# Kernel tuning notes

Measured on AMD Instinct MI355X. Metric: run time of the kernel, lower is better.

The kernel has to match this reference:

```python
import jax, jax.numpy as jnp
import numpy as np

N = 100000   # nodes
E = 1600000  # edges
IN = 32      # in_channels
H = 64       # hidden_channels
L = 16       # latent_dim
G = 64       # graphs in batch


def setup_inputs() -> dict:
    key = jax.random.key(0)
    ks = jax.random.split(key, 20)
    def w(k, shape, fan):
        return jax.random.normal(k, shape, jnp.float32) * (1.0 / np.sqrt(fan))
    inp = {}
    inp["x"] = jax.random.normal(ks[0], (N, IN), jnp.float32)
    inp["edge_index"] = jax.random.randint(ks[1], (2, E), 0, N)
    inp["batch"] = jnp.sort(jax.random.randint(ks[2], (N,), 0, G))
    # encoder GCN convs: in->h, h->h, h->h
    inp["W_enc0"] = w(ks[3], (IN, H), IN); inp["b_enc0"] = jnp.zeros((H,), jnp.float32)
    inp["W_enc1"] = w(ks[4], (H, H), H);   inp["b_enc1"] = jnp.zeros((H,), jnp.float32)
    inp["W_enc2"] = w(ks[5], (H, H), H);   inp["b_enc2"] = jnp.zeros((H,), jnp.float32)
    # latent projection and decoder projection
    inp["W_proj"] = w(ks[6], (H, L), H);   inp["b_proj"] = jnp.zeros((L,), jnp.float32)
    inp["W_dec_proj"] = w(ks[7], (L, H), L); inp["b_dec_proj"] = jnp.zeros((H,), jnp.float32)
    # decoder GCN convs: h->h, h->in
    inp["W_dec0"] = w(ks[8], (H, H), H);   inp["b_dec0"] = jnp.zeros((H,), jnp.float32)
    inp["W_dec1"] = w(ks[9], (H, IN), H);  inp["b_dec1"] = jnp.zeros((IN,), jnp.float32)
    return inp


def gcn_conv(x, W, b, src, dst, dinv):
    xw = x @ W                                   # [N, out]
    coef = (dinv[src] * dinv[dst])[:, None]      # [E, 1]
    out = jax.ops.segment_sum(xw[src] * coef, dst, num_segments=N)
    out = out + xw * (dinv * dinv)[:, None]      # self-loop contribution
    return out + b


def reference(x, edge_index, batch,
              W_enc0, b_enc0, W_enc1, b_enc1, W_enc2, b_enc2,
              W_proj, b_proj, W_dec_proj, b_dec_proj,
              W_dec0, b_dec0, W_dec1, b_dec1):
    src, dst = edge_index[0], edge_index[1]
    # degree with self-loops (computed on target nodes, PyG default)
    deg = jax.ops.segment_sum(jnp.ones((E,), jnp.float32), dst, num_segments=N) + 1.0
    dinv = jax.lax.rsqrt(deg)
    # encoder (eval mode: dropout is identity)
    h = jax.nn.relu(gcn_conv(x, W_enc0, b_enc0, src, dst, dinv))
    h = jax.nn.relu(gcn_conv(h, W_enc1, b_enc1, src, dst, dinv))
    h = jax.nn.relu(gcn_conv(h, W_enc2, b_enc2, src, dst, dinv))
    # global mean pool over graph ids
    sums = jax.ops.segment_sum(h, batch, num_segments=G)
    cnt = jax.ops.segment_sum(jnp.ones((N,), jnp.float32), batch, num_segments=G)
    g = sums / jnp.maximum(cnt, 1.0)[:, None]    # [G, H]
    z = g @ W_proj + b_proj                      # [G, L]
    # decoder: broadcast z back to nodes, project, two GCN convs
    d = jax.nn.relu(z[batch] @ W_dec_proj + b_dec_proj)
    d = jax.nn.relu(gcn_conv(d, W_dec0, b_dec0, src, dst, dinv))
    x_recon = gcn_conv(d, W_dec1, b_dec1, src, dst, dinv)
    return (x_recon, z)
```

## Files before the change

kernel.cpp:

```cpp
#include <hip/hip_runtime.h>
#include <hip/hip_bf16.h>

typedef unsigned long long u64;

static constexpr int IN_CH  = 32;
static constexpr int HID    = 64;
static constexpr int LAT    = 16;
static constexpr int NGRAPH = 64;
static constexpr int CPB8   = 8;
static constexpr int CPB4   = 4;


__device__ inline void add4(float4& a, const float4& b) {
    a.x += b.x; a.y += b.y; a.z += b.z; a.w += b.w;
}


__global__ __launch_bounds__(256) void bhist_kernel(const int* __restrict__ ei,
                                                    int* __restrict__ bh, int E) {
    __shared__ int lh[256];
    lh[threadIdx.x] = 0;
    __syncthreads();
    int base = blockIdx.x * 2048;
    #pragma unroll
    for (int j = 0; j < 8; j++) {
        int idx = base + j * 256 + threadIdx.x;
        if (idx < E) atomicAdd(&lh[ei[E + idx] >> 9], 1);
    }
    __syncthreads();
    if (lh[threadIdx.x]) atomicAdd(&bh[threadIdx.x], lh[threadIdx.x]);
}


__global__ __launch_bounds__(256) void bin_kernel(
        const int* __restrict__ ei, const int* __restrict__ bh,
        int* __restrict__ gcur, u64* __restrict__ sout, int E) {
    __shared__ int lhist[256], lscan[256], lcur[256], gbase[256], bbaseL[256];
    __shared__ u64 sbuf[2048];
    int tid = threadIdx.x;
    lhist[tid] = 0;
    {
        int v = bh[tid];
        lscan[tid] = v;
        for (int off = 1; off < 256; off <<= 1) {
            __syncthreads();
            int x = (tid >= off) ? lscan[tid - off] : 0;
            __syncthreads();
            lscan[tid] += x;
        }
        __syncthreads();
        bbaseL[tid] = lscan[tid] - v;
    }
    __syncthreads();
    int base = blockIdx.x * 2048;
    int cnt = min(2048, E - base);
    int myb[8]; u64 myp[8];
    #pragma unroll
    for (int j = 0; j < 8; j++) {
        int idx = base + j * 256 + tid;
        myb[j] = -1;
        if (idx < E) {
            int key = ei[E + idx], val = ei[idx];
            int b = key >> 9;
            myb[j] = b;
            myp[j] = ((u64)(unsigned)key << 32) | (unsigned)val;
            atomicAdd(&lhist[b], 1);
        }
    }
    __syncthreads();
    int v = lhist[tid];
    lscan[tid] = v;
    for (int off = 1; off < 256; off <<= 1) {
        __syncthreads();
        int x = (tid >= off) ? lscan[tid - off] : 0;
        __syncthreads();
        lscan[tid] += x;
    }
    __syncthreads();
    int excl = lscan[tid] - v;
    __syncthreads();
    lscan[tid] = excl;
    lcur[tid] = excl;
    __syncthreads();
    #pragma unroll
    for (int j = 0; j < 8; j++) {
        if (myb[j] >= 0) {
            int pos = atomicAdd(&lcur[myb[j]], 1);
            sbuf[pos] = myp[j];
        }
    }
    gbase[tid] = v ? atomicAdd(&gcur[tid], v) : 0;
    __syncthreads();
    for (int i = tid; i < cnt; i += 256) {
        u64 p = sbuf[i];
        int b = (int)(p >> 41);
        sout[bbaseL[b] + gbase[b] + (i - lscan[b])] = p;
    }
}


__global__ __launch_bounds__(256) void degb_kernel(
        const u64* __restrict__ staged, const int* __restrict__ bh,
        const int* __restrict__ batch,
        int* __restrict__ rank, int* __restrict__ perm, int* __restrict__ cnt2,
        int* __restrict__ rowptr2, float* __restrict__ dinvR,
        float2* __restrict__ pgR, int* __restrict__ bbase, int N, int E) {
    __shared__ int sc[256];
    __shared__ int ldeg[512], lrank[512], degS[512], psum[512];
    __shared__ int kcur[256];
    __shared__ int s0s, s1s;
    int b = blockIdx.x, tid = threadIdx.x;
    {
        int bv = bh[tid];
        sc[tid] = bv;
        for (int off = 1; off < 256; off <<= 1) {
            __syncthreads();
            int x = (tid >= off) ? sc[tid - off] : 0;
            __syncthreads();
            sc[tid] += x;
        }
        __syncthreads();
        if (tid == b) { s0s = sc[tid] - bv; s1s = sc[tid]; }
    }
    ldeg[tid] = 0; ldeg[tid + 256] = 0;
    degS[tid] = 0; degS[tid + 256] = 0;
    kcur[tid] = 0;
    __syncthreads();
    int s0 = s0s, s1 = s1s;
    int base = b << 9;
    for (int i = s0 + tid; i < s1; i += 256)
        atomicAdd(&ldeg[(int)(__builtin_nontemporal_load(&staged[i]) >> 32) - base], 1);
    __syncthreads();
    int k = N - base; k = k < 0 ? 0 : (k > 512 ? 512 : k);
    #pragma unroll
    for (int j = 0; j < 2; j++) {
        int t = tid + j * 256;
        if (t < k) atomicAdd(&kcur[min(ldeg[t], 255)], 1);
    }
    __syncthreads();
    {
        int hv = kcur[tid];
        sc[tid] = hv;
        for (int off = 1; off < 256; off <<= 1) {
            __syncthreads();
            int x = (tid >= off) ? sc[tid - off] : 0;
            __syncthreads();
            sc[tid] += x;
        }
        __syncthreads();
        kcur[tid] = sc[tid] - hv;
    }
    __syncthreads();
    #pragma unroll
    for (int j = 0; j < 2; j++) {
        int t = tid + j * 256;
        if (t < k) lrank[t] = atomicAdd(&kcur[min(ldeg[t], 255)], 1);
    }
    __syncthreads();
    #pragma unroll
    for (int j = 0; j < 2; j++) {
        int t = tid + j * 256;
        if (t < k) degS[lrank[t]] = ldeg[t];
    }
    __syncthreads();
    {
        int v0 = degS[2 * tid], v1 = degS[2 * tid + 1];
        int T = v0 + v1;
        sc[tid] = T;
        for (int off = 1; off < 256; off <<= 1) {
            __syncthreads();
            int x = (tid >= off) ? sc[tid - off] : 0;
            __syncthreads();
            sc[tid] += x;
        }
        __syncthreads();
        int ex = sc[tid] - T;
        psum[2 * tid] = ex;
        psum[2 * tid + 1] = ex + v0;
    }
    __syncthreads();
    #pragma unroll
    for (int j = 0; j < 2; j++) {
        int t = tid + j * 256;
        if (t < k) {
            int n = base + t;
            int d = ldeg[t], lr = lrank[t];
            int r = base + lr;
            rank[n] = r;
            perm[r] = n;
            cnt2[r] = d;
            rowptr2[r] = s0 + psum[lr];
            float dv = rsqrtf((float)d + 1.0f);
            dinvR[r] = dv;
            pgR[r] = make_float2(dv, __int_as_float(batch[n]));
        }
    }
    if (tid == 0) {
        bbase[b] = s0;
        if (b == 255) bbase[256] = E;
    }
}


__global__ __launch_bounds__(256) void csr_kernel(
        const u64* __restrict__ staged, const int* __restrict__ bbase,
        const int* __restrict__ rank, const int* __restrict__ rowptr2,
        int* __restrict__ col) {
    __shared__ int lcur[512];
    int b = blockIdx.x, tid = threadIdx.x;
    lcur[tid] = 0; lcur[tid + 256] = 0;
    __syncthreads();
    int s0 = bbase[b], s1 = bbase[b + 1];
    int base = b << 9;
    for (int i = s0 + tid; i < s1; i += 256) {
        u64 p = __builtin_nontemporal_load(&staged[i]);
        int dst = (int)(p >> 32);
        int src = (int)(p & 0xffffffffu);
        int rd = rank[dst];
        int pos = rowptr2[rd] + atomicAdd(&lcur[rd - base], 1);
        col[pos] = rank[src];
    }
}


__global__ void slice_x_kernel(const float* __restrict__ x, const int* __restrict__ perm,
                               const float* __restrict__ dinvR,
                               float* __restrict__ xs, int N) {
    int idx = blockIdx.x * 256 + threadIdx.x;
    if (idx >= N * 4) return;
    int r = idx >> 2, h = idx & 3;
    int sl = blockIdx.y;
    int n = perm[r];
    float4 v = ((const float4*)x)[(size_t)n * 8 + sl * 4 + h];
    float dn = dinvR[r];
    v.x *= dn; v.y *= dn; v.z *= dn; v.w *= dn;
    ((float4*)(xs + (size_t)sl * N * 16))[idx] = v;
}


template <int C, bool ADD_BIAS, bool OUT_ROWMAJOR>
__global__ __launch_bounds__(256) void agg_kernel(
        const float* __restrict__ in, float* __restrict__ out,
        const int* __restrict__ rowptr2, const int* __restrict__ cnt2,
        const int* __restrict__ col, const float* __restrict__ dinvR,
        const int* __restrict__ perm, const float* __restrict__ bias,
        int nbk, int N) {
    constexpr int NSL = C / 16;
    int sl = blockIdx.x % NSL;
    int o  = blockIdx.x / NSL;
    int chunk = (o % nbk) * CPB8 + (o / nbk);
    int quad = threadIdx.x >> 2, q = threadIdx.x & 3;
    int r = chunk * 64 + quad;
    if (r >= N) return;
    const float4* inS = (const float4*)(in + (size_t)sl * N * 16);
    int start = rowptr2[r], m = cnt2[r];
    const int* cp = col + start;
    float4 acc0 = inS[(size_t)r * 4 + q];
    float4 acc1 = make_float4(0.f, 0.f, 0.f, 0.f);
    int i = 0;
    for (; i + 8 <= m; i += 8) {
        int4 ca = *(const int4*)(cp + i);
        int4 cb = *(const int4*)(cp + i + 4);
        float4 v0 = inS[(size_t)ca.x*4+q], v1 = inS[(size_t)ca.y*4+q];
        float4 v2 = inS[(size_t)ca.z*4+q], v3 = inS[(size_t)ca.w*4+q];
        float4 v4 = inS[(size_t)cb.x*4+q], v5 = inS[(size_t)cb.y*4+q];
        float4 v6 = inS[(size_t)cb.z*4+q], v7 = inS[(size_t)cb.w*4+q];
        add4(v0, v1); add4(v2, v3); add4(v4, v5); add4(v6, v7);
        add4(v0, v2); add4(v4, v6);
        add4(acc0, v0); add4(acc1, v4);
    }
    if (i + 4 <= m) {
        int4 ca = *(const int4*)(cp + i);
        float4 v0 = inS[(size_t)ca.x*4+q], v1 = inS[(size_t)ca.y*4+q];
        float4 v2 = inS[(size_t)ca.z*4+q], v3 = inS[(size_t)ca.w*4+q];
        add4(v0, v1); add4(v2, v3); add4(v0, v2);
        add4(acc0, v0);
        i += 4;
    }
    for (; i < m; ++i) {
        int c = cp[i];
        add4(acc1, inS[(size_t)c * 4 + q]);
    }
    add4(acc0, acc1);
    float dn = dinvR[r];
    acc0.x *= dn; acc0.y *= dn; acc0.z *= dn; acc0.w *= dn;
    if (ADD_BIAS) {
        float4 b4 = ((const float4*)bias)[sl * 4 + q];
        add4(acc0, b4);
    }
    if (OUT_ROWMAJOR) ((float4*)out)[(size_t)perm[r] * (C / 4) + sl * 4 + q] = acc0;
    else ((float4*)(out + (size_t)sl * N * 16))[(size_t)r * 4 + q] = acc0;
}


__global__ __launch_bounds__(256) void gagg_kernel(
        const float* __restrict__ dg, const float2* __restrict__ pgR,
        const int* __restrict__ rowptr2, const int* __restrict__ cnt2,
        const int* __restrict__ col, float* __restrict__ out, int nbk, int N) {
    __shared__ float dgL[NGRAPH * 68];
    for (int i = threadIdx.x; i < NGRAPH * 64; i += 256)
        dgL[(i >> 6) * 68 + (i & 63)] = dg[i];
    __syncthreads();
    int slot = threadIdx.x >> 1, e = threadIdx.x & 1;
    int o = blockIdx.x;
    int chunk = (o % nbk) * CPB4 + (o / nbk);
    int r = chunk * 128 + slot;
    if (r >= N) return;
    const float4* dgL4 = (const float4*)dgL;
    int start = rowptr2[r], m = cnt2[r];
    const int* cp = col + start;
    float2 ps = pgR[r];
    float dn = ps.x;
    int gs = __float_as_int(ps.y);
    float4 acc[8];
    {
        const float4* rp = dgL4 + gs * 17 + e * 8;
        #pragma unroll
        for (int j = 0; j < 8; ++j) {
            float4 v = rp[j];
            acc[j] = make_float4(dn * v.x, dn * v.y, dn * v.z, dn * v.w);
        }
    }
    int i = 0;
    for (; i + 4 <= m; i += 4) {
        int4 ca = *(const int4*)(cp + i);
        float2 p0 = pgR[ca.x], p1 = pgR[ca.y], p2 = pgR[ca.z], p3 = pgR[ca.w];
        const float4* r0 = dgL4 + __float_as_int(p0.y) * 17 + e * 8;
        const float4* r1 = dgL4 + __float_as_int(p1.y) * 17 + e * 8;
        const float4* r2 = dgL4 + __float_as_int(p2.y) * 17 + e * 8;
        const float4* r3 = dgL4 + __float_as_int(p3.y) * 17 + e * 8;
        float w0 = p0.x, w1 = p1.x, w2 = p2.x, w3 = p3.x;
        #pragma unroll
        for (int j = 0; j < 8; ++j) {
            float4 v0 = r0[j], v1 = r1[j], v2 = r2[j], v3 = r3[j];
            acc[j].x += (w0 * v0.x + w1 * v1.x) + (w2 * v2.x + w3 * v3.x);
            acc[j].y += (w0 * v0.y + w1 * v1.y) + (w2 * v2.y + w3 * v3.y);
            acc[j].z += (w0 * v0.z + w1 * v1.z) + (w2 * v2.z + w3 * v3.z);
            acc[j].w += (w0 * v0.w + w1 * v1.w) + (w2 * v2.w + w3 * v3.w);
        }
    }
    for (; i < m; ++i) {
        int c0 = cp[i];
        float2 p0 = pgR[c0];
        const float4* r0 = dgL4 + __float_as_int(p0.y) * 17 + e * 8;
        float w0 = p0.x;
        #pragma unroll
        for (int j = 0; j < 8; ++j) {
            float4 v0 = r0[j];
            acc[j].x += w0 * v0.x; acc[j].y += w0 * v0.y;
            acc[j].z += w0 * v0.z; acc[j].w += w0 * v0.w;
        }
    }
    #pragma unroll
    for (int k = 0; k < 4; ++k) {
        #pragma unroll
        for (int jj = 0; jj < 2; ++jj) {
            float4 v = acc[k * 2 + jj];
            v.x *= dn; v.y *= dn; v.z *= dn; v.w *= dn;
            int ch = e * 32 + k * 8 + jj * 4;
            ((float4*)(out + (size_t)(ch >> 4) * N * 16))[(size_t)r * 4 + ((ch & 15) >> 2)] = v;
        }
    }
}


template <int CIN, int COUT, bool RELU, bool BIAS, bool SCALE, bool OUT_ROWMAJOR>
__global__ __launch_bounds__(256) void gemm_kernel(
        const float* __restrict__ in, const float* __restrict__ W,
        const float* __restrict__ b, const float* __restrict__ dinvR,
        const int* __restrict__ perm, float* __restrict__ out, int N) {
    constexpr int NPB = 256 / COUT;
    constexpr int K4 = CIN / 4;
    __shared__ float4 xsh[NPB * K4];
    int r  = threadIdx.x / COUT;
    int co = threadIdx.x % COUT;
    float w[CIN];
    #pragma unroll
    for (int k = 0; k < CIN; ++k) w[k] = W[k * COUT + co];
    float bsv = BIAS ? b[co] : 0.f;
    int ngroups = (N + NPB - 1) / NPB;
    for (int grp = blockIdx.x; grp < ngroups; grp += gridDim.x) {
        int base = grp * NPB;
        __syncthreads();
        for (int i = threadIdx.x; i < NPB * K4; i += 256) {
            int rr = i / K4, k4 = i % K4;
            int n = base + rr;
            float4 v = make_float4(0.f, 0.f, 0.f, 0.f);
            if (n < N) v = ((const float4*)(in + (size_t)(k4 >> 2) * N * 16))[(size_t)n * 4 + (k4 & 3)];
            xsh[i] = v;
        }
        __syncthreads();
        int n = base + r;
        if (n < N) {
            float acc = bsv;
            #pragma unroll
            for (int k4 = 0; k4 < K4; ++k4) {
                float4 xv = xsh[r * K4 + k4];
                acc += xv.x * w[4 * k4] + xv.y * w[4 * k4 + 1]
                     + xv.z * w[4 * k4 + 2] + xv.w * w[4 * k4 + 3];
            }
            if (RELU) acc = fmaxf(acc, 0.f);
            if (SCALE) acc *= dinvR[n];
            if (OUT_ROWMAJOR) out[(size_t)perm[n] * COUT + co] = acc;
            else out[(size_t)(co >> 4) * N * 16 + (size_t)n * 16 + (co & 15)] = acc;
        }
    }
}


__global__ __launch_bounds__(256) void gemm2_kernel(
        const float* __restrict__ in, const float* __restrict__ W0,
        const float* __restrict__ b0, const float* __restrict__ W1,
        const float* __restrict__ dinvR, float* __restrict__ out, int N) {
    constexpr int NPB = 4;
    __shared__ float4 xsh[NPB * 16];
    __shared__ float t1sh[NPB * 65];
    __shared__ float w1sh[HID * IN_CH];
    int tid = threadIdx.x;
    int r  = tid >> 6;
    int co = tid & 63;
    float w0[HID];
    #pragma unroll
    for (int k = 0; k < HID; ++k) w0[k] = W0[k * HID + co];
    float b0v = b0[co];
    for (int i = tid; i < HID * IN_CH; i += 256) w1sh[i] = W1[i];
    int r2  = tid >> 5;
    int co2 = tid & 31;
    int ngroups = (N + NPB - 1) / NPB;
    for (int grp = blockIdx.x; grp < ngroups; grp += gridDim.x) {
        int base = grp * NPB;
        __syncthreads();
        if (tid < NPB * 16) {
            int rr = tid >> 4, k4 = tid & 15;
            int n = base + rr;
            float4 v = make_float4(0.f, 0.f, 0.f, 0.f);
            if (n < N) v = ((const float4*)(in + (size_t)(k4 >> 2) * N * 16))[(size_t)n * 4 + (k4 & 3)];
            xsh[tid] = v;
        }
        __syncthreads();
        {
            float acc = b0v;
            #pragma unroll
            for (int k4 = 0; k4 < 16; ++k4) {
                float4 xv = xsh[r * 16 + k4];
                acc += xv.x * w0[4 * k4] + xv.y * w0[4 * k4 + 1]
                     + xv.z * w0[4 * k4 + 2] + xv.w * w0[4 * k4 + 3];
            }
            t1sh[r * 65 + co] = fmaxf(acc, 0.f);
        }
        __syncthreads();
        if (r2 < NPB) {
            int n = base + r2;
            if (n < N) {
                float acc = 0.f;
                #pragma unroll
                for (int k = 0; k < HID; ++k)
                    acc += t1sh[r2 * 65 + k] * w1sh[k * IN_CH + co2];
                acc *= dinvR[n];
                out[(size_t)(co2 >> 4) * N * 16 + (size_t)n * 16 + (co2 & 15)] = acc;
            }
        }
    }
}


__global__ __launch_bounds__(256) void pool_kernel(
        const float* __restrict__ h, const int* __restrict__ batch,
        float* __restrict__ sums, int* __restrict__ cntb, int N) {
    const int CHUNK = 512;
    int chunkStart = blockIdx.x * CHUNK;
    int c = threadIdx.x & 63;
    int r = threadIdx.x >> 6;
    int curg = -1;
    float acc = 0.f;
    int cnt = 0;
    int end = chunkStart + CHUNK;
    if (end > N) end = N;
    for (int n = chunkStart + r; n < end; n += 4) {
        int g = batch[n];
        if (g != curg) {
            if (curg >= 0) {
                atomicAdd(&sums[curg * 64 + c], acc);
                if (c == 0) atomicAdd(&cntb[curg], cnt);
            }
            curg = g; acc = 0.f; cnt = 0;
        }
        acc += h[(size_t)n * 64 + c];
        cnt++;
    }
    if (curg >= 0) {
        atomicAdd(&sums[curg * 64 + c], acc);
        if (c == 0) atomicAdd(&cntb[curg], cnt);
    }
}


__global__ __launch_bounds__(1024) void latent_kernel(
        const float* __restrict__ sums, const int* __restrict__ cntb,
        const float* __restrict__ Wp, const float* __restrict__ bp,
        const float* __restrict__ Wd, const float* __restrict__ bd,
        float* __restrict__ z_out, float* __restrict__ dg) {
    __shared__ float zl[NGRAPH * LAT];
    int t = threadIdx.x;
    {
        int g = t / LAT, l = t % LAT;
        float cf = (float)cntb[g];
        float inv = 1.0f / fmaxf(cf, 1.0f);
        float acc = bp[l];
        #pragma unroll
        for (int k = 0; k < HID; k++) acc += sums[g * HID + k] * inv * Wp[k * LAT + l];
        zl[t] = acc;
        z_out[t] = acc;
    }
    __syncthreads();
    #pragma unroll
    for (int i = 0; i < 4; i++) {
        int idx = t + i * 1024;
        int g = idx >> 6, c = idx & 63;
        float acc = bd[c];
        #pragma unroll
        for (int l = 0; l < LAT; l++) acc += zl[g * LAT + l] * Wd[l * HID + c];
        dg[idx] = fmaxf(acc, 0.f);
    }
}


extern "C" void kernel_launch(void* const* d_in, const int* in_sizes, int n_in,
                              void* d_out, int out_size, void* d_ws, size_t ws_size,
                              hipStream_t stream) {
    const float* x          = (const float*)d_in[0];
    const int*   ei         = (const int*)d_in[1];
    const int*   batch      = (const int*)d_in[2];
    const float* W_enc0     = (const float*)d_in[3];
    const float* b_enc0     = (const float*)d_in[4];
    const float* W_enc1     = (const float*)d_in[5];
    const float* b_enc1     = (const float*)d_in[6];
    const float* W_enc2     = (const float*)d_in[7];
    const float* b_enc2     = (const float*)d_in[8];
    const float* W_proj     = (const float*)d_in[9];
    const float* b_proj     = (const float*)d_in[10];
    const float* W_dec_proj = (const float*)d_in[11];
    const float* b_dec_proj = (const float*)d_in[12];
    const float* W_dec0     = (const float*)d_in[13];
    const float* b_dec0     = (const float*)d_in[14];
    const float* W_dec1     = (const float*)d_in[15];
    const float* b_dec1     = (const float*)d_in[16];

    const int N = in_sizes[0] / IN_CH;
    const int E = in_sizes[1] / 2;

    char* ws = (char*)d_ws;
    size_t off = 0;
    auto alloc = [&](size_t bytes) {
        void* p = ws + off;
        off += (bytes + 255) & ~(size_t)255;
        return p;
    };
    float* A       = (float*)alloc((size_t)N * HID * 4);
    float* B       = (float*)alloc((size_t)N * HID * 4);
    float* XS      = (float*)alloc((size_t)N * IN_CH * 4);
    int*   col     = (int*)  alloc((size_t)E * 4);
    int*   cnt2    = (int*)  alloc((size_t)N * 4);
    int*   rowptr2 = (int*)  alloc((size_t)(N + 1) * 4);
    int*   perm    = (int*)  alloc((size_t)N * 4);
    int*   rank    = (int*)  alloc((size_t)N * 4);
    float* dinvR   = (float*)alloc((size_t)N * 4);
    float2* pgR    = (float2*)alloc((size_t)N * 8);
    int*   bbase   = (int*)  alloc(257 * 4);
    char* zbase = ws + off;
    int*   bh      = (int*)  alloc(256 * 4);
    int*   gcurD   = (int*)  alloc(256 * 4);
    float* sums    = (float*)alloc((size_t)NGRAPH * HID * 4);
    int*   cntb    = (int*)  alloc((size_t)NGRAPH * 4);
    size_t zbytes = (size_t)((ws + off) - zbase);
    float* dg      = (float*)alloc((size_t)NGRAPH * HID * 4);

    u64* staged1 = (u64*)XS;

    float* x_recon = (float*)d_out;
    float* z_out   = (float*)d_out + (size_t)N * IN_CH;

    hipMemsetAsync(zbase, 0, zbytes, stream);

    int ebins = (E + 2047) / 2048;
    int nbk = (N + 511) >> 9;
    int chunks8 = nbk * CPB8;
    int chunks4 = nbk * CPB4;

    bhist_kernel<<<ebins, 256, 0, stream>>>(ei, bh, E);
    bin_kernel<<<ebins, 256, 0, stream>>>(ei, bh, gcurD, staged1, E);
    degb_kernel<<<256, 256, 0, stream>>>(staged1, bh, batch, rank, perm, cnt2,
                                         rowptr2, dinvR, pgR, bbase, N, E);
    csr_kernel<<<256, 256, 0, stream>>>(staged1, bbase, rank, rowptr2, col);

    {
        dim3 g((N * 4 + 255) / 256, IN_CH / 16);
        slice_x_kernel<<<g, 256, 0, stream>>>(x, perm, dinvR, XS, N);
    }

    agg_kernel<IN_CH, false, false><<<chunks8 * 2, 256, 0, stream>>>(
        XS, A, rowptr2, cnt2, col, dinvR, perm, nullptr, nbk, N);
    gemm_kernel<IN_CH, HID, true, true, true, false><<<2048, 256, 0, stream>>>(
        A, W_enc0, b_enc0, dinvR, perm, B, N);
    agg_kernel<HID, false, false><<<chunks8 * 4, 256, 0, stream>>>(
        B, A, rowptr2, cnt2, col, dinvR, perm, nullptr, nbk, N);
    gemm_kernel<HID, HID, true, true, true, false><<<2048, 256, 0, stream>>>(
        A, W_enc1, b_enc1, dinvR, perm, B, N);
    agg_kernel<HID, false, false><<<chunks8 * 4, 256, 0, stream>>>(
        B, A, rowptr2, cnt2, col, dinvR, perm, nullptr, nbk, N);
    gemm_kernel<HID, HID, true, true, false, true><<<2048, 256, 0, stream>>>(
        A, W_enc2, b_enc2, dinvR, perm, B, N);

    pool_kernel<<<(N + 511) / 512, 256, 0, stream>>>(B, batch, sums, cntb, N);
    latent_kernel<<<1, 1024, 0, stream>>>(sums, cntb, W_proj, b_proj, W_dec_proj, b_dec_proj, z_out, dg);

    gagg_kernel<<<chunks4, 256, 0, stream>>>(dg, pgR, rowptr2, cnt2, col, A, nbk, N);
    gemm2_kernel<<<2048, 256, 0, stream>>>(A, W_dec0, b_dec0, W_dec1, dinvR, B, N);
    agg_kernel<IN_CH, true, true><<<chunks8 * 2, 256, 0, stream>>>(
        B, x_recon, rowptr2, cnt2, col, dinvR, perm, b_dec1, nbk, N);
}
```

Before: 603.3 us.

## Pack staged edges into 32 bits and fuse last encoder GEMM with pooling

Staged edge pairs are packed into 32 bits (9-bit local destination plus 17-bit source) instead of 64, halving staging traffic in the bin, degree and CSR kernels. The final encoder GEMM now accumulates its ReLU output directly into per-graph sums in shared memory, so the full hidden matrix is never written and re-read by a separate pool kernel. Graph counts are computed by binary search over the sorted batch array. The packing assumes node ids below 2^17, and the pooled sums now use float atomics in rank order, which changes summation order.

Measured after the change: 600.8 us. Within noise of the previous version (-0.4%).

```diff
diff --git a/kernel.cpp b/kernel.cpp
--- a/kernel.cpp
+++ b/kernel.cpp
@@ -2,6 +2,7 @@
 #include <hip/hip_bf16.h>
 
 typedef unsigned long long u64;
+typedef unsigned int u32;
 
 static constexpr int IN_CH  = 32;
 static constexpr int HID    = 64;
@@ -34,7 +35,7 @@
 
 __global__ __launch_bounds__(256) void bin_kernel(
         const int* __restrict__ ei, const int* __restrict__ bh,
-        int* __restrict__ gcur, u64* __restrict__ sout, int E) {
+        int* __restrict__ gcur, u32* __restrict__ sout, int E) {
     __shared__ int lhist[256], lscan[256], lcur[256], gbase[256], bbaseL[256];
     __shared__ u64 sbuf[2048];
     int tid = threadIdx.x;
@@ -63,7 +64,8 @@
             int key = ei[E + idx], val = ei[idx];
             int b = key >> 9;
             myb[j] = b;
-            myp[j] = ((u64)(unsigned)key << 32) | (unsigned)val;
+            u32 packed = ((u32)(key & 511) << 17) | (u32)val;
+            myp[j] = ((u64)(unsigned)b << 32) | packed;
             atomicAdd(&lhist[b], 1);
         }
     }
@@ -93,14 +95,14 @@
     __syncthreads();
     for (int i = tid; i < cnt; i += 256) {
         u64 p = sbuf[i];
-        int b = (int)(p >> 41);
-        sout[bbaseL[b] + gbase[b] + (i - lscan[b])] = p;
+        int b = (int)(p >> 32);
+        sout[bbaseL[b] + gbase[b] + (i - lscan[b])] = (u32)(p & 0xffffffffu);
     }
 }
 
 
 __global__ __launch_bounds__(256) void degb_kernel(
-        const u64* __restrict__ staged, const int* __restrict__ bh,
+        const u32* __restrict__ staged, const int* __restrict__ bh,
         const int* __restrict__ batch,
         int* __restrict__ rank, int* __restrict__ perm, int* __restrict__ cnt2,
         int* __restrict__ rowptr2, float* __restrict__ dinvR,
@@ -129,7 +131,7 @@
     int s0 = s0s, s1 = s1s;
     int base = b << 9;
     for (int i = s0 + tid; i < s1; i += 256)
-        atomicAdd(&ldeg[(int)(__builtin_nontemporal_load(&staged[i]) >> 32) - base], 1);
+        atomicAdd(&ldeg[(int)(__builtin_nontemporal_load(&staged[i]) >> 17)], 1);
     __syncthreads();
     int k = N - base; k = k < 0 ? 0 : (k > 512 ? 512 : k);
     #pragma unroll
@@ -203,7 +205,7 @@
 
 
 __global__ __launch_bounds__(256) void csr_kernel(
-        const u64* __restrict__ staged, const int* __restrict__ bbase,
+        const u32* __restrict__ staged, const int* __restrict__ bbase,
         const int* __restrict__ rank, const int* __restrict__ rowptr2,
         int* __restrict__ col) {
     __shared__ int lcur[512];
@@ -213,13 +215,25 @@
     int s0 = bbase[b], s1 = bbase[b + 1];
     int base = b << 9;
     for (int i = s0 + tid; i < s1; i += 256) {
-        u64 p = __builtin_nontemporal_load(&staged[i]);
-        int dst = (int)(p >> 32);
-        int src = (int)(p & 0xffffffffu);
-        int rd = rank[dst];
+        u32 p = __builtin_nontemporal_load(&staged[i]);
+        int low9 = (int)(p >> 17);
+        int src  = (int)(p & 0x1FFFFu);
+        int rd = rank[base + low9];
         int pos = rowptr2[rd] + atomicAdd(&lcur[rd - base], 1);
         col[pos] = rank[src];
     }
+}
+
+
+__global__ void cntb_kernel(const int* __restrict__ batch, int* __restrict__ cntb, int N) {
+    int g = threadIdx.x;
+    if (g >= NGRAPH) return;
+    auto lb = [&](int key) {
+        int lo = 0, hi = N;
+        while (lo < hi) { int mid = (lo + hi) >> 1; if (batch[mid] < key) lo = mid + 1; else hi = mid; }
+        return lo;
+    };
+    cntb[g] = lb(g + 1) - lb(g);
 }
 
 
@@ -408,29 +422,27 @@
 }
 
 
-__global__ __launch_bounds__(256) void gemm2_kernel(
-        const float* __restrict__ in, const float* __restrict__ W0,
-        const float* __restrict__ b0, const float* __restrict__ W1,
-        const float* __restrict__ dinvR, float* __restrict__ out, int N) {
+__global__ __launch_bounds__(256) void gemm_pool_kernel(
+        const float* __restrict__ in, const float* __restrict__ W,
+        const float* __restrict__ b, const float2* __restrict__ pgR,
+        float* __restrict__ sums, int N) {
     constexpr int NPB = 4;
-    __shared__ float4 xsh[NPB * 16];
-    __shared__ float t1sh[NPB * 65];
-    __shared__ float w1sh[HID * IN_CH];
+    constexpr int K4 = HID / 4;
+    __shared__ float4 xsh[NPB * K4];
+    __shared__ float lsum[NGRAPH * HID];
     int tid = threadIdx.x;
     int r  = tid >> 6;
     int co = tid & 63;
-    float w0[HID];
-    #pragma unroll
-    for (int k = 0; k < HID; ++k) w0[k] = W0[k * HID + co];
-    float b0v = b0[co];
-    for (int i = tid; i < HID * IN_CH; i += 256) w1sh[i] = W1[i];
-    int r2  = tid >> 5;
-    int co2 = tid & 31;
+    float w[HID];
+    #pragma unroll
+    for (int k = 0; k < HID; ++k) w[k] = W[k * HID + co];
+    float bv = b[co];
+    for (int i = tid; i < NGRAPH * HID; i += 256) lsum[i] = 0.f;
     int ngroups = (N + NPB - 1) / NPB;
     for (int grp = blockIdx.x; grp < ngroups; grp += gridDim.x) {
         int base = grp * NPB;
         __syncthreads();
-        if (tid < NPB * 16) {
+        if (tid < NPB * K4) {
             int rr = tid >> 4, k4 = tid & 15;
             int n = base + rr;
             float4 v = make_float4(0.f, 0.f, 0.f, 0.f);
@@ -438,59 +450,24 @@
             xsh[tid] = v;
         }
         __syncthreads();
-        {
-            float acc = b0v;
+        int n = base + r;
+        if (n < N) {
+            float acc = bv;
             #pragma unroll
-            for (int k4 = 0; k4 < 16; ++k4) {
-                float4 xv = xsh[r * 16 + k4];
-                acc += xv.x * w0[4 * k4] + xv.y * w0[4 * k4 + 1]
-                     + xv.z * w0[4 * k4 + 2] + xv.w * w0[4 * k4 + 3];
+            for (int k4 = 0; k4 < K4; ++k4) {
+                float4 xv = xsh[r * K4 + k4];
+                acc += xv.x * w[4 * k4] + xv.y * w[4 * k4 + 1]
+                     + xv.z * w[4 * k4 + 2] + xv.w * w[4 * k4 + 3];
             }
-            t1sh[r * 65 + co] = fmaxf(acc, 0.f);
-        }
-        __syncthreads();
-        if (r2 < NPB) {
-            int n = base + r2;
-            if (n < N) {
-                float acc = 0.f;
-                #pragma unroll
-                for (int k = 0; k < HID; ++k)
-                    acc += t1sh[r2 * 65 + k] * w1sh[k * IN_CH + co2];
-                acc *= dinvR[n];
-                out[(size_t)(co2 >> 4) * N * 16 + (size_t)n * 16 + (co2 & 15)] = acc;
-            }
-        }
-    }
-}
-
-
-__global__ __launch_bounds__(256) void pool_kernel(
-        const float* __restrict__ h, const int* __restrict__ batch,
-        float* __restrict__ sums, int* __restrict__ cntb, int N) {
-    const int CHUNK = 512;
-    int chunkStart = blockIdx.x * CHUNK;
-    int c = threadIdx.x & 63;
-    int r = threadIdx.x >> 6;
-    int curg = -1;
-    float acc = 0.f;
-    int cnt = 0;
-    int end = chunkStart + CHUNK;
-    if (end > N) end = N;
-    for (int n = chunkStart + r; n < end; n += 4) {
-        int g = batch[n];
-        if (g != curg) {
-            if (curg >= 0) {
-                atomicAdd(&sums[curg * 64 + c], acc);
-                if (c == 0) atomicAdd(&cntb[curg], cnt);
-            }
-            curg = g; acc = 0.f; cnt = 0;
-        }
-        acc += h[(size_t)n * 64 + c];
-        cnt++;
-    }
-    if (curg >= 0) {
-        atomicAdd(&sums[curg * 64 + c], acc);
-        if (c == 0) atomicAdd(&cntb[curg], cnt);
+            acc = fmaxf(acc, 0.f);
+            int g = __float_as_int(pgR[n].y);
+            atomicAdd(&lsum[g * HID + co], acc);
+        }
+    }
+    __syncthreads();
+    for (int i = tid; i < NGRAPH * HID; i += 256) {
+        float v = lsum[i];
+        if (v != 0.f) atomicAdd(&sums[i], v);
     }
 }
 
@@ -521,6 +498,62 @@
         #pragma unroll
         for (int l = 0; l < LAT; l++) acc += zl[g * LAT + l] * Wd[l * HID + c];
         dg[idx] = fmaxf(acc, 0.f);
+    }
+}
+
+
+__global__ __launch_bounds__(256) void gemm2_kernel(
+        const float* __restrict__ in, const float* __restrict__ W0,
+        const float* __restrict__ b0, const float* __restrict__ W1,
+        const float* __restrict__ dinvR, float* __restrict__ out, int N) {
+    constexpr int NPB = 4;
+    __shared__ float4 xsh[NPB * 16];
+    __shared__ float t1sh[NPB * 65];
+    __shared__ float w1sh[HID * IN_CH];
+    int tid = threadIdx.x;
+    int r  = tid >> 6;
+    int co = tid & 63;
+    float w0[HID];
+    #pragma unroll
+    for (int k = 0; k < HID; ++k) w0[k] = W0[k * HID + co];
+    float b0v = b0[co];
+    for (int i = tid; i < HID * IN_CH; i += 256) w1sh[i] = W1[i];
+    int r2  = tid >> 5;
+    int co2 = tid & 31;
+    int ngroups = (N + NPB - 1) / NPB;
+    for (int grp = blockIdx.x; grp < ngroups; grp += gridDim.x) {
+        int base = grp * NPB;
+        __syncthreads();
+        if (tid < NPB * 16) {
+            int rr = tid >> 4, k4 = tid & 15;
+            int n = base + rr;
+            float4 v = make_float4(0.f, 0.f, 0.f, 0.f);
+            if (n < N) v = ((const float4*)(in + (size_t)(k4 >> 2) * N * 16))[(size_t)n * 4 + (k4 & 3)];
+            xsh[tid] = v;
+        }
+        __syncthreads();
+        {
+            float acc = b0v;
+            #pragma unroll
+            for (int k4 = 0; k4 < 16; ++k4) {
+                float4 xv = xsh[r * 16 + k4];
+                acc += xv.x * w0[4 * k4] + xv.y * w0[4 * k4 + 1]
+                     + xv.z * w0[4 * k4 + 2] + xv.w * w0[4 * k4 + 3];
+            }
+            t1sh[r * 65 + co] = fmaxf(acc, 0.f);
+        }
+        __syncthreads();
+        if (r2 < NPB) {
+            int n = base + r2;
+            if (n < N) {
+                float acc = 0.f;
+                #pragma unroll
+                for (int k = 0; k < HID; ++k)
+                    acc += t1sh[r2 * 65 + k] * w1sh[k * IN_CH + co2];
+                acc *= dinvR[n];
+                out[(size_t)(co2 >> 4) * N * 16 + (size_t)n * 16 + (co2 & 15)] = acc;
+            }
+        }
     }
 }
 
@@ -575,7 +608,7 @@
     size_t zbytes = (size_t)((ws + off) - zbase);
     float* dg      = (float*)alloc((size_t)NGRAPH * HID * 4);
 
-    u64* staged1 = (u64*)XS;
+    u32* staged1 = (u32*)XS;
 
     float* x_recon = (float*)d_out;
     float* z_out   = (float*)d_out + (size_t)N * IN_CH;
@@ -592,6 +625,7 @@
     degb_kernel<<<256, 256, 0, stream>>>(staged1, bh, batch, rank, perm, cnt2,
                                          rowptr2, dinvR, pgR, bbase, N, E);
     csr_kernel<<<256, 256, 0, stream>>>(staged1, bbase, rank, rowptr2, col);
+    cntb_kernel<<<1, 64, 0, stream>>>(batch, cntb, N);
 
     {
         dim3 g((N * 4 + 255) / 256, IN_CH / 16);
@@ -608,10 +642,8 @@
         A, W_enc1, b_enc1, dinvR, perm, B, N);
     agg_kernel<HID, false, false><<<chunks8 * 4, 256, 0, stream>>>(
         B, A, rowptr2, cnt2, col, dinvR, perm, nullptr, nbk, N);
-    gemm_kernel<HID, HID, true, true, false, true><<<2048, 256, 0, stream>>>(
-        A, W_enc2, b_enc2, dinvR, perm, B, N);
-
-    pool_kernel<<<(N + 511) / 512, 256, 0, stream>>>(B, batch, sums, cntb, N);
+    gemm_pool_kernel<<<512, 256, 0, stream>>>(A, W_enc2, b_enc2, pgR, sums, N);
+
     latent_kernel<<<1, 1024, 0, stream>>>(sums, cntb, W_proj, b_proj, W_dec_proj, b_dec_proj, z_out, dg);
 
     gagg_kernel<<<chunks4, 256, 0, stream>>>(dg, pgR, rowptr2, cnt2, col, A, nbk, N);
```
